# Kernel tuning notes

Measured on AMD Instinct MI355X. Metric: run time of the kernel, lower is better.

The kernel has to match this reference:

```python
import jax, jax.numpy as jnp
import numpy as np

HEADS = 4
DIM_HEAD = 128


def setup_inputs() -> dict:
    key = jax.random.key(0)
    k1, k2, k3, k4 = jax.random.split(key, 4)
    B, C, H, W = 8, 256, 64, 64
    hidden = HEADS * DIM_HEAD  # 512
    x = jax.random.normal(k1, (B, C, H, W), dtype=jnp.float32)
    # 1x1 convs are just channel matmuls; store kernels as [out_ch, in_ch]
    w_qkv = jax.random.normal(k2, (3 * hidden, C), dtype=jnp.float32) * 0.05
    w_out = jax.random.normal(k3, (C, hidden), dtype=jnp.float32) * 0.05
    b_out = jax.random.normal(k4, (C,), dtype=jnp.float32) * 0.05
    return {"x": x, "w_qkv": w_qkv, "w_out": w_out, "b_out": b_out}


def reference(x, w_qkv, w_out, b_out):
    B, C, H, W = x.shape
    n = H * W
    # to_qkv: 1x1 conv without bias == channel matmul
    qkv = jnp.einsum('bchw,oc->bohw', x, w_qkv)  # [B, 3*heads*dim_head, H, W]
    qkv = qkv.reshape(B, 3, HEADS, DIM_HEAD, n)  # 'b (qkv heads c) h w -> b qkv heads c n'
    q, k, v = qkv[:, 0], qkv[:, 1], qkv[:, 2]    # each [B, heads, dim_head, n]
    k = jax.nn.softmax(k, axis=-1)               # softmax over spatial positions
    context = jnp.einsum('bhdn,bhen->bhde', k, v)   # [B, heads, d, e]
    out = jnp.einsum('bhde,bhdn->bhen', context, q)  # [B, heads, e, n]
    out = out.reshape(B, HEADS * DIM_HEAD, H, W)
    # to_out: 1x1 conv with bias
    return jnp.einsum('bchw,oc->bohw', out, w_out) + b_out[None, :, None, None]
```

## Files before the change

### kernel.cpp

```cpp
#include <hip/hip_runtime.h>
#include <stdint.h>


using frag8 = __attribute__((ext_vector_type(8))) short;
using f32x4 = __attribute__((ext_vector_type(4))) float;

__device__ __forceinline__ float bf2f(unsigned short u) {
    union { unsigned int u; float f; } c;
    c.u = ((unsigned int)u) << 16;
    return c.f;
}
__device__ __forceinline__ unsigned short f2bf(float f) {
    union { float f; unsigned int u; } c; c.f = f;
    unsigned int u = c.u;
    return (unsigned short)((u + 0x7FFFu + ((u >> 16) & 1u)) >> 16);
}

__device__ __forceinline__ void gl_lds16(const void* g, void* l) {
    __builtin_amdgcn_global_load_lds(
        (const __attribute__((address_space(1))) unsigned int*)g,
        (__attribute__((address_space(3))) unsigned int*)l, 16, 0, 0);
}

__global__ __launch_bounds__(256) void k0_weights(
    const float* __restrict__ w_qkv, const float* __restrict__ w_out,
    unsigned short* __restrict__ wkvb, unsigned short* __restrict__ woutb,
    unsigned short* __restrict__ wqT)
{
    __shared__ float T[64][65];
    const int blk = blockIdx.x;
    const int tid = threadIdx.x;
    if (blk < 256) {
        const int idx = (blk * 256 + tid) * 4;
        float4 v = *(const float4*)(w_qkv + 512 * 256 + idx);
        ushort4 o;
        o.x = f2bf(v.x); o.y = f2bf(v.y); o.z = f2bf(v.z); o.w = f2bf(v.w);
        *(ushort4*)(wkvb + idx) = o;
    } else if (blk < 384) {
        const int idx = ((blk - 256) * 256 + tid) * 4;
        float4 v = *(const float4*)(w_out + idx);
        ushort4 o;
        o.x = f2bf(v.x); o.y = f2bf(v.y); o.z = f2bf(v.z); o.w = f2bf(v.w);
        *(ushort4*)(woutb + idx) = o;
    } else {
        const int t = blk - 384;
        const int j0 = (t >> 2) * 64, c0 = (t & 3) * 64;
        const int r = tid >> 4, cc = (tid & 15) * 4;
        #pragma unroll
        for (int p = 0; p < 4; ++p) {
            float4 v = *(const float4*)(w_qkv + (j0 + r + p * 16) * 256 + c0 + cc);
            T[r + p * 16][cc + 0] = v.x; T[r + p * 16][cc + 1] = v.y;
            T[r + p * 16][cc + 2] = v.z; T[r + p * 16][cc + 3] = v.w;
        }
        __syncthreads();
        const int c = tid >> 2, jj = (tid & 3) * 16;
        #pragma unroll
        for (int g = 0; g < 4; ++g) {
            ushort4 o;
            o.x = f2bf(T[jj + g * 4 + 0][c]);
            o.y = f2bf(T[jj + g * 4 + 1][c]);
            o.z = f2bf(T[jj + g * 4 + 2][c]);
            o.w = f2bf(T[jj + g * 4 + 3][c]);
            *(ushort4*)(wqT + (c0 + c) * 512 + j0 + jj + g * 4) = o;
        }
    }
}

__global__ __launch_bounds__(256) void k0_xt(
    const float* __restrict__ x, unsigned short* __restrict__ xbT)
{
    __shared__ float T[64][65];
    const int tid = threadIdx.x;
    const int n0 = blockIdx.x * 64, c0 = blockIdx.y * 64, b = blockIdx.z;
    const float* xb = x + (size_t)b * 1048576;
    const int cr = tid >> 4, nc = (tid & 15) * 4;
    #pragma unroll
    for (int p = 0; p < 4; ++p) {
        float4 v = *(const float4*)(xb + (size_t)(c0 + cr + p * 16) * 4096 + n0 + nc);
        T[cr + p * 16][nc + 0] = v.x; T[cr + p * 16][nc + 1] = v.y;
        T[cr + p * 16][nc + 2] = v.z; T[cr + p * 16][nc + 3] = v.w;
    }
    __syncthreads();
    const int n = tid >> 2, cc = (tid & 3) * 16;
    unsigned short* dst = xbT + (size_t)b * 1048576 + (size_t)(n0 + n) * 256 + c0 + cc;
    #pragma unroll
    for (int g = 0; g < 4; ++g) {
        ushort4 o;
        o.x = f2bf(T[cc + g * 4 + 0][n]);
        o.y = f2bf(T[cc + g * 4 + 1][n]);
        o.z = f2bf(T[cc + g * 4 + 2][n]);
        o.w = f2bf(T[cc + g * 4 + 3][n]);
        *(ushort4*)(dst + g * 4) = o;
    }
}

template<int MODE>
__global__ __launch_bounds__(256) void mfma_bt(
    const unsigned short* __restrict__ A0, int lda,
    const unsigned short* __restrict__ B0, int ldb,
    void* __restrict__ C0, int ldc,
    const float* __restrict__ bias, int Kp,
    unsigned long long sAz, unsigned long long sBz, unsigned long long sCz)
{
    __shared__ unsigned short As[128 * 32];
    __shared__ unsigned short Bs[128 * 32];
    const int tid  = threadIdx.x;
    const int w    = tid >> 6, lane = tid & 63;
    const int quad = lane >> 4, l16 = lane & 15;
    const int wm = (w >> 1) * 64, wn = (w & 1) * 64;
    const int z = blockIdx.z;

    const unsigned short* A;
    const unsigned short* B;
    int ks, ke, m0, n0;
    if constexpr (MODE == 2) {
        m0 = 0; n0 = 0;
        ks = blockIdx.x * 512; ke = ks + 512;
        const unsigned long long off =
            ((unsigned long long)(z >> 2) * 1024ull + (unsigned long long)(z & 3) * 128ull) * 4096ull;
        A = A0 + off; B = B0 + off;
    } else if constexpr (MODE == 3) {
        m0 = blockIdx.y * 128; n0 = 0;
        ks = 0; ke = Kp;
        A = A0 + (unsigned long long)(z & 3) * 128ull + (unsigned long long)m0 * lda;
        B = B0 + (unsigned long long)z * 16384ull;
    } else {
        m0 = blockIdx.y * 128; n0 = blockIdx.x * 128;
        ks = 0; ke = Kp;
        A = A0 + sAz * z + (unsigned long long)m0 * lda;
        B = B0 + sBz * z + (unsigned long long)n0 * ldb;
    }

    const int cA0 = w * 128 + lane;
    const int cA1 = cA0 + 64;
    const unsigned short* gA0 = A + (unsigned long long)(cA0 >> 2) * lda + (cA0 & 3) * 8;
    const unsigned short* gA1 = A + (unsigned long long)(cA1 >> 2) * lda + (cA1 & 3) * 8;
    const unsigned short* gB0 = B + (unsigned long long)(cA0 >> 2) * ldb + (cA0 & 3) * 8;
    const unsigned short* gB1 = B + (unsigned long long)(cA1 >> 2) * ldb + (cA1 & 3) * 8;
    unsigned short* lA0 = As + w * 1024;
    unsigned short* lA1 = As + w * 1024 + 512;
    unsigned short* lB0 = Bs + w * 1024;
    unsigned short* lB1 = Bs + w * 1024 + 512;

    f32x4 acc[4][4] = {};

    for (int k0 = ks; k0 < ke; k0 += 32) {
        gl_lds16(gA0 + k0, lA0);
        gl_lds16(gA1 + k0, lA1);
        gl_lds16(gB0 + k0, lB0);
        gl_lds16(gB1 + k0, lB1);
        __syncthreads();
        frag8 a[4], b[4];
        #pragma unroll
        for (int t = 0; t < 4; ++t) {
            a[t] = *(const frag8*)(As + (wm + t * 16 + l16) * 32 + quad * 8);
            b[t] = *(const frag8*)(Bs + (wn + t * 16 + l16) * 32 + quad * 8);
        }
        #pragma unroll
        for (int mt = 0; mt < 4; ++mt)
            #pragma unroll
            for (int nt = 0; nt < 4; ++nt)
                acc[mt][nt] = __builtin_amdgcn_mfma_f32_16x16x32_bf16(
                    a[mt], b[nt], acc[mt][nt], 0, 0, 0);
        __syncthreads();
    }

    if constexpr (MODE == 0 || MODE == 3) {
        unsigned short* C;
        if constexpr (MODE == 0)
            C = (unsigned short*)C0 + sCz * z + (unsigned long long)m0 * ldc + n0;
        else
            C = (unsigned short*)C0 + (unsigned long long)(z >> 2) * 131072ull
              + (unsigned long long)(z & 3) * 128ull + (unsigned long long)m0 * ldc;
        #pragma unroll
        for (int mt = 0; mt < 4; ++mt) {
            const int row = wm + mt * 16 + quad * 4;
            #pragma unroll
            for (int nt = 0; nt < 4; ++nt) {
                const int col = wn + nt * 16 + l16;
                #pragma unroll
                for (int r = 0; r < 4; ++r)
                    C[(unsigned long long)(row + r) * ldc + col] = f2bf(acc[mt][nt][r]);
            }
        }
    } else if constexpr (MODE == 4) {
        unsigned short* C = (unsigned short*)C0 + sCz * z + (unsigned long long)m0 * ldc + n0;
        if (blockIdx.y < 4) {
            float* rs = (float*)bias;
            #pragma unroll
            for (int mt = 0; mt < 4; ++mt) {
                const int row = wm + mt * 16 + quad * 4;
                float rsum[4] = {0.f, 0.f, 0.f, 0.f};
                #pragma unroll
                for (int nt = 0; nt < 4; ++nt) {
                    const int col = wn + nt * 16 + l16;
                    #pragma unroll
                    for (int r = 0; r < 4; ++r) {
                        float e = __expf(acc[mt][nt][r]);
                        rsum[r] += e;
                        C[(unsigned long long)(row + r) * ldc + col] = f2bf(e);
                    }
                }
                #pragma unroll
                for (int r = 0; r < 4; ++r) {
                    float v = rsum[r];
                    v += __shfl_xor(v, 1, 64);
                    v += __shfl_xor(v, 2, 64);
                    v += __shfl_xor(v, 4, 64);
                    v += __shfl_xor(v, 8, 64);
                    if (l16 == 0)
                        atomicAdd(rs + (unsigned long long)z * 512 + m0 + row + r, v);
                }
            }
        } else {
            #pragma unroll
            for (int mt = 0; mt < 4; ++mt) {
                const int row = wm + mt * 16 + quad * 4;
                #pragma unroll
                for (int nt = 0; nt < 4; ++nt) {
                    const int col = wn + nt * 16 + l16;
                    #pragma unroll
                    for (int r = 0; r < 4; ++r)
                        C[(unsigned long long)(row + r) * ldc + col] = f2bf(acc[mt][nt][r]);
                }
            }
        }
    } else if constexpr (MODE == 1) {
        float* C = (float*)C0 + sCz * z + (unsigned long long)m0 * ldc + n0;
        const float* bp = bias + m0;
        #pragma unroll
        for (int mt = 0; mt < 4; ++mt) {
            const int row = wm + mt * 16 + quad * 4;
            #pragma unroll
            for (int nt = 0; nt < 4; ++nt) {
                const int col = wn + nt * 16 + l16;
                #pragma unroll
                for (int r = 0; r < 4; ++r)
                    C[(unsigned long long)(row + r) * ldc + col] = acc[mt][nt][r] + bp[row + r];
            }
        }
    } else {
        float* C = (float*)C0 + (unsigned long long)z * 16384ull;
        #pragma unroll
        for (int mt = 0; mt < 4; ++mt) {
            const int row = wm + mt * 16 + quad * 4;
            #pragma unroll
            for (int nt = 0; nt < 4; ++nt) {
                const int col = wn + nt * 16 + l16;
                #pragma unroll
                for (int r = 0; r < 4; ++r)
                    atomicAdd(C + (row + r) * 128 + col, acc[mt][nt][r]);
            }
        }
    }
}

__global__ __launch_bounds__(256) void k3_scale(
    const float* __restrict__ ctx, const float* __restrict__ rowsum,
    unsigned short* __restrict__ ctxb)
{
    const int idx = (blockIdx.x * 256 + threadIdx.x) * 4;
    const float inv = 1.0f / rowsum[idx >> 7];
    float4 t = *(const float4*)(ctx + idx);
    ushort4 o;
    o.x = f2bf(t.x * inv); o.y = f2bf(t.y * inv);
    o.z = f2bf(t.z * inv); o.w = f2bf(t.w * inv);
    *(ushort4*)(ctxb + idx) = o;
}

extern "C" void kernel_launch(void* const* d_in, const int* in_sizes, int n_in,
                              void* d_out, int out_size, void* d_ws, size_t ws_size,
                              hipStream_t stream) {
    (void)in_sizes; (void)n_in; (void)out_size; (void)ws_size;
    const float* x     = (const float*)d_in[0];
    const float* w_qkv = (const float*)d_in[1];
    const float* w_out = (const float*)d_in[2];
    const float* b_out = (const float*)d_in[3];
    float* out = (float*)d_out;

    char* ws = (char*)d_ws;
    unsigned short* kv     = (unsigned short*)ws;
    unsigned short* xbT    = (unsigned short*)(ws + 67108864);
    unsigned short* wkvb   = (unsigned short*)(ws + 83886080);
    unsigned short* woutb  = (unsigned short*)(ws + 84410368);
    unsigned short* wqT    = (unsigned short*)(ws + 84672512);
    float*          ctx    = (float*)(ws + 84934656);
    float*          rowsum = (float*)(ws + 87031808);
    unsigned short* ctxb   = (unsigned short*)(ws + 87048192);
    unsigned short* Mb     = (unsigned short*)(ws + 88096768);
    unsigned short* Nb     = (unsigned short*)(ws + 90193920);

    hipMemsetAsync(ws + 84934656, 0, 2097152 + 16384, stream);

    k0_weights<<<dim3(416), 256, 0, stream>>>(w_qkv, w_out, wkvb, woutb, wqT);
    k0_xt<<<dim3(64, 4, 8), 256, 0, stream>>>(x, xbT);
    mfma_bt<4><<<dim3(32, 8, 8), 256, 0, stream>>>(
        wkvb, 256, xbT, 256, kv, 4096, rowsum, 256,
        0ull, 1048576ull, 4194304ull);
    mfma_bt<2><<<dim3(8, 1, 32), 256, 0, stream>>>(
        kv, 4096, kv + (size_t)512 * 4096, 4096, ctx, 128, nullptr, 0,
        0ull, 0ull, 0ull);
    k3_scale<<<dim3(512), 256, 0, stream>>>(ctx, rowsum, ctxb);
    mfma_bt<3><<<dim3(1, 2, 32), 256, 0, stream>>>(
        woutb, 512, ctxb, 128, Mb, 512, nullptr, 128,
        0ull, 0ull, 0ull);
    mfma_bt<0><<<dim3(2, 2, 8), 256, 0, stream>>>(
        Mb, 512, wqT, 512, Nb, 256, nullptr, 512,
        131072ull, 0ull, 65536ull);
    mfma_bt<1><<<dim3(32, 2, 8), 256, 0, stream>>>(
        Nb, 256, xbT, 256, out, 4096, b_out, 256,
        65536ull, 1048576ull, 1048576ull);
}
```

Measured before the change: 190.9 us.

## Fuse K/V projection, exp and context GEMM into one kernel; swizzle LDS

Replaces the separate K/V projection kernel (which wrote a 64MB bf16 kv buffer) and the context GEMM with a fused kernel. Each block computes exp(K) and V tiles for 128 spatial positions into LDS, then accumulates K·V^T directly, atomically adding partial context and row sums. It also adds an XOR swizzle to the LDS tile layout in the generic GEMM to reduce bank conflicts. The aim is to remove the large global round trip of kv. In exchange, the fused kernel uses 80KB of LDS, which limits occupancy, and each block recomputes its weight tiles.

After: 200.5 us. 1.05x slower.

```diff
diff --git a/kernel.cpp b/kernel.cpp
--- a/kernel.cpp
+++ b/kernel.cpp
@@ -5,11 +5,6 @@
 using frag8 = __attribute__((ext_vector_type(8))) short;
 using f32x4 = __attribute__((ext_vector_type(4))) float;
 
-__device__ __forceinline__ float bf2f(unsigned short u) {
-    union { unsigned int u; float f; } c;
-    c.u = ((unsigned int)u) << 16;
-    return c.f;
-}
 __device__ __forceinline__ unsigned short f2bf(float f) {
     union { float f; unsigned int u; } c; c.f = f;
     unsigned int u = c.u;
@@ -112,31 +107,24 @@
 
     const unsigned short* A;
     const unsigned short* B;
-    int ks, ke, m0, n0;
-    if constexpr (MODE == 2) {
-        m0 = 0; n0 = 0;
-        ks = blockIdx.x * 512; ke = ks + 512;
-        const unsigned long long off =
-            ((unsigned long long)(z >> 2) * 1024ull + (unsigned long long)(z & 3) * 128ull) * 4096ull;
-        A = A0 + off; B = B0 + off;
-    } else if constexpr (MODE == 3) {
+    int m0, n0;
+    if constexpr (MODE == 3) {
         m0 = blockIdx.y * 128; n0 = 0;
-        ks = 0; ke = Kp;
         A = A0 + (unsigned long long)(z & 3) * 128ull + (unsigned long long)m0 * lda;
         B = B0 + (unsigned long long)z * 16384ull;
     } else {
         m0 = blockIdx.y * 128; n0 = blockIdx.x * 128;
-        ks = 0; ke = Kp;
         A = A0 + sAz * z + (unsigned long long)m0 * lda;
         B = B0 + sBz * z + (unsigned long long)n0 * ldb;
     }
 
-    const int cA0 = w * 128 + lane;
-    const int cA1 = cA0 + 64;
-    const unsigned short* gA0 = A + (unsigned long long)(cA0 >> 2) * lda + (cA0 & 3) * 8;
-    const unsigned short* gA1 = A + (unsigned long long)(cA1 >> 2) * lda + (cA1 & 3) * 8;
-    const unsigned short* gB0 = B + (unsigned long long)(cA0 >> 2) * ldb + (cA0 & 3) * 8;
-    const unsigned short* gB1 = B + (unsigned long long)(cA1 >> 2) * ldb + (cA1 & 3) * 8;
+    const int c0 = w * 128 + lane, c1 = c0 + 64;
+    const int r0 = c0 >> 2, g0 = ((c0 & 3) ^ ((r0 >> 1) & 3)) * 8;
+    const int r1 = c1 >> 2, g1 = ((c1 & 3) ^ ((r1 >> 1) & 3)) * 8;
+    const unsigned short* gA0 = A + (unsigned long long)r0 * lda + g0;
+    const unsigned short* gA1 = A + (unsigned long long)r1 * lda + g1;
+    const unsigned short* gB0 = B + (unsigned long long)r0 * ldb + g0;
+    const unsigned short* gB1 = B + (unsigned long long)r1 * ldb + g1;
     unsigned short* lA0 = As + w * 1024;
     unsigned short* lA1 = As + w * 1024 + 512;
     unsigned short* lB0 = Bs + w * 1024;
@@ -144,7 +132,7 @@
 
     f32x4 acc[4][4] = {};
 
-    for (int k0 = ks; k0 < ke; k0 += 32) {
+    for (int k0 = 0; k0 < Kp; k0 += 32) {
         gl_lds16(gA0 + k0, lA0);
         gl_lds16(gA1 + k0, lA1);
         gl_lds16(gB0 + k0, lB0);
@@ -153,8 +141,10 @@
         frag8 a[4], b[4];
         #pragma unroll
         for (int t = 0; t < 4; ++t) {
-            a[t] = *(const frag8*)(As + (wm + t * 16 + l16) * 32 + quad * 8);
-            b[t] = *(const frag8*)(Bs + (wn + t * 16 + l16) * 32 + quad * 8);
+            const int ra = wm + t * 16 + l16;
+            const int rb = wn + t * 16 + l16;
+            a[t] = *(const frag8*)(As + ra * 32 + ((quad ^ ((ra >> 1) & 3)) << 3));
+            b[t] = *(const frag8*)(Bs + rb * 32 + ((quad ^ ((rb >> 1) & 3)) << 3));
         }
         #pragma unroll
         for (int mt = 0; mt < 4; ++mt)
@@ -183,74 +173,159 @@
                     C[(unsigned long long)(row + r) * ldc + col] = f2bf(acc[mt][nt][r]);
             }
         }
-    } else if constexpr (MODE == 4) {
-        unsigned short* C = (unsigned short*)C0 + sCz * z + (unsigned long long)m0 * ldc + n0;
-        if (blockIdx.y < 4) {
-            float* rs = (float*)bias;
-            #pragma unroll
-            for (int mt = 0; mt < 4; ++mt) {
-                const int row = wm + mt * 16 + quad * 4;
-                float rsum[4] = {0.f, 0.f, 0.f, 0.f};
-                #pragma unroll
-                for (int nt = 0; nt < 4; ++nt) {
-                    const int col = wn + nt * 16 + l16;
+    } else {
+        float* C = (float*)C0 + sCz * z + (unsigned long long)m0 * ldc + n0;
+        const float* bp = bias + m0;
+        #pragma unroll
+        for (int mt = 0; mt < 4; ++mt) {
+            const int row = wm + mt * 16 + quad * 4;
+            #pragma unroll
+            for (int nt = 0; nt < 4; ++nt) {
+                const int col = wn + nt * 16 + l16;
+                #pragma unroll
+                for (int r = 0; r < 4; ++r)
+                    C[(unsigned long long)(row + r) * ldc + col] = acc[mt][nt][r] + bp[row + r];
+            }
+        }
+    }
+}
+
+__global__ __launch_bounds__(256) void k13_ctx(
+    const unsigned short* __restrict__ wkvb,
+    const unsigned short* __restrict__ xbT,
+    float* __restrict__ ctx, float* __restrict__ rowsum)
+{
+    __shared__ unsigned short As[128 * 32];
+    __shared__ unsigned short Bs[128 * 32];
+    __shared__ unsigned short Kt[128 * 128];
+    __shared__ unsigned short Vt[128 * 128];
+    const int tid  = threadIdx.x;
+    const int w    = tid >> 6, lane = tid & 63;
+    const int quad = lane >> 4, l16 = lane & 15;
+    const int wm = (w >> 1) * 64, wn = (w & 1) * 64;
+    const int s = blockIdx.x, h = blockIdx.y, b = blockIdx.z;
+
+    const unsigned short* Wk = wkvb + (size_t)(h * 128) * 256;
+    const unsigned short* Wv = wkvb + (size_t)(512 + h * 128) * 256;
+    const unsigned short* Xb = xbT + (size_t)b * 1048576;
+
+    const int c0 = w * 128 + lane, c1 = c0 + 64;
+    const int r0 = c0 >> 2, g0 = ((c0 & 3) ^ ((r0 >> 1) & 3)) * 8;
+    const int r1 = c1 >> 2, g1 = ((c1 & 3) ^ ((r1 >> 1) & 3)) * 8;
+    unsigned short* lA0 = As + w * 1024;
+    unsigned short* lA1 = As + w * 1024 + 512;
+    unsigned short* lB0 = Bs + w * 1024;
+    unsigned short* lB1 = Bs + w * 1024 + 512;
+
+    float rsum[4][4] = {};
+    f32x4 ctxa[4][4] = {};
+
+    for (int ch = 0; ch < 2; ++ch) {
+        const unsigned short* X0 = Xb + (size_t)(blockIdx.x * 256 + ch * 128) * 256;
+
+        #pragma unroll 1
+        for (int g = 0; g < 2; ++g) {
+            const unsigned short* Wg = g ? Wv : Wk;
+            f32x4 acc[4][4] = {};
+            for (int k0 = 0; k0 < 256; k0 += 32) {
+                gl_lds16(Wg + (size_t)r0 * 256 + g0 + k0, lA0);
+                gl_lds16(Wg + (size_t)r1 * 256 + g1 + k0, lA1);
+                gl_lds16(X0 + (size_t)r0 * 256 + g0 + k0, lB0);
+                gl_lds16(X0 + (size_t)r1 * 256 + g1 + k0, lB1);
+                __syncthreads();
+                frag8 a[4], bb[4];
+                #pragma unroll
+                for (int t = 0; t < 4; ++t) {
+                    const int ra = wm + t * 16 + l16;
+                    const int rb = wn + t * 16 + l16;
+                    a[t]  = *(const frag8*)(As + ra * 32 + ((quad ^ ((ra >> 1) & 3)) << 3));
+                    bb[t] = *(const frag8*)(Bs + rb * 32 + ((quad ^ ((rb >> 1) & 3)) << 3));
+                }
+                #pragma unroll
+                for (int mt = 0; mt < 4; ++mt)
                     #pragma unroll
-                    for (int r = 0; r < 4; ++r) {
-                        float e = __expf(acc[mt][nt][r]);
-                        rsum[r] += e;
-                        C[(unsigned long long)(row + r) * ldc + col] = f2bf(e);
+                    for (int nt = 0; nt < 4; ++nt)
+                        acc[mt][nt] = __builtin_amdgcn_mfma_f32_16x16x32_bf16(
+                            a[mt], bb[nt], acc[mt][nt], 0, 0, 0);
+                __syncthreads();
+            }
+            unsigned short* T = g ? Vt : Kt;
+            if (g == 0) {
+                #pragma unroll
+                for (int mt = 0; mt < 4; ++mt) {
+                    const int row = wm + mt * 16 + quad * 4;
+                    #pragma unroll
+                    for (int nt = 0; nt < 4; ++nt) {
+                        const int col = wn + nt * 16 + l16;
+                        #pragma unroll
+                        for (int r = 0; r < 4; ++r) {
+                            float e = __expf(acc[mt][nt][r]);
+                            rsum[mt][r] += e;
+                            T[((row + r) * 128 + col) ^ (((row + r) & 7) << 3)] = f2bf(e);
+                        }
                     }
                 }
-                #pragma unroll
-                for (int r = 0; r < 4; ++r) {
-                    float v = rsum[r];
-                    v += __shfl_xor(v, 1, 64);
-                    v += __shfl_xor(v, 2, 64);
-                    v += __shfl_xor(v, 4, 64);
-                    v += __shfl_xor(v, 8, 64);
-                    if (l16 == 0)
-                        atomicAdd(rs + (unsigned long long)z * 512 + m0 + row + r, v);
+            } else {
+                #pragma unroll
+                for (int mt = 0; mt < 4; ++mt) {
+                    const int row = wm + mt * 16 + quad * 4;
+                    #pragma unroll
+                    for (int nt = 0; nt < 4; ++nt) {
+                        const int col = wn + nt * 16 + l16;
+                        #pragma unroll
+                        for (int r = 0; r < 4; ++r)
+                            T[((row + r) * 128 + col) ^ (((row + r) & 7) << 3)] =
+                                f2bf(acc[mt][nt][r]);
+                    }
                 }
             }
-        } else {
-            #pragma unroll
-            for (int mt = 0; mt < 4; ++mt) {
-                const int row = wm + mt * 16 + quad * 4;
-                #pragma unroll
-                for (int nt = 0; nt < 4; ++nt) {
-                    const int col = wn + nt * 16 + l16;
-                    #pragma unroll
-                    for (int r = 0; r < 4; ++r)
-                        C[(unsigned long long)(row + r) * ldc + col] = f2bf(acc[mt][nt][r]);
-                }
-            }
-        }
-    } else if constexpr (MODE == 1) {
-        float* C = (float*)C0 + sCz * z + (unsigned long long)m0 * ldc + n0;
-        const float* bp = bias + m0;
-        #pragma unroll
-        for (int mt = 0; mt < 4; ++mt) {
-            const int row = wm + mt * 16 + quad * 4;
-            #pragma unroll
-            for (int nt = 0; nt < 4; ++nt) {
-                const int col = wn + nt * 16 + l16;
-                #pragma unroll
-                for (int r = 0; r < 4; ++r)
-                    C[(unsigned long long)(row + r) * ldc + col] = acc[mt][nt][r] + bp[row + r];
-            }
-        }
-    } else {
-        float* C = (float*)C0 + (unsigned long long)z * 16384ull;
-        #pragma unroll
-        for (int mt = 0; mt < 4; ++mt) {
-            const int row = wm + mt * 16 + quad * 4;
-            #pragma unroll
-            for (int nt = 0; nt < 4; ++nt) {
-                const int col = wn + nt * 16 + l16;
-                #pragma unroll
-                for (int r = 0; r < 4; ++r)
-                    atomicAdd(C + (row + r) * 128 + col, acc[mt][nt][r]);
-            }
+        }
+        __syncthreads();
+
+        #pragma unroll
+        for (int kk = 0; kk < 4; ++kk) {
+            frag8 a[4], bb[4];
+            #pragma unroll
+            for (int t = 0; t < 4; ++t) {
+                const int ra = wm + t * 16 + l16;
+                const int rb = wn + t * 16 + l16;
+                a[t]  = *(const frag8*)(Kt + ((ra * 128 + kk * 32 + quad * 8) ^ ((ra & 7) << 3)));
+                bb[t] = *(const frag8*)(Vt + ((rb * 128 + kk * 32 + quad * 8) ^ ((rb & 7) << 3)));
+            }
+            #pragma unroll
+            for (int mt = 0; mt < 4; ++mt)
+                #pragma unroll
+                for (int nt = 0; nt < 4; ++nt)
+                    ctxa[mt][nt] = __builtin_amdgcn_mfma_f32_16x16x32_bf16(
+                        a[mt], bb[nt], ctxa[mt][nt], 0, 0, 0);
+        }
+        __syncthreads();
+    }
+
+    float* cp = ctx + (size_t)(b * 4 + h) * 16384ull;
+    #pragma unroll
+    for (int mt = 0; mt < 4; ++mt) {
+        const int row = wm + mt * 16 + quad * 4;
+        #pragma unroll
+        for (int nt = 0; nt < 4; ++nt) {
+            const int col = wn + nt * 16 + l16;
+            #pragma unroll
+            for (int r = 0; r < 4; ++r)
+                atomicAdd(cp + (row + r) * 128 + col, ctxa[mt][nt][r]);
+        }
+    }
+    float* rs = rowsum + b * 512 + h * 128;
+    #pragma unroll
+    for (int mt = 0; mt < 4; ++mt) {
+        const int row = wm + mt * 16 + quad * 4;
+        #pragma unroll
+        for (int r = 0; r < 4; ++r) {
+            float v = rsum[mt][r];
+            v += __shfl_xor(v, 1, 64);
+            v += __shfl_xor(v, 2, 64);
+            v += __shfl_xor(v, 4, 64);
+            v += __shfl_xor(v, 8, 64);
+            if (l16 == 0) atomicAdd(rs + row + r, v);
         }
     }
 }
@@ -279,27 +354,21 @@
     float* out = (float*)d_out;
 
     char* ws = (char*)d_ws;
-    unsigned short* kv     = (unsigned short*)ws;
-    unsigned short* xbT    = (unsigned short*)(ws + 67108864);
-    unsigned short* wkvb   = (unsigned short*)(ws + 83886080);
-    unsigned short* woutb  = (unsigned short*)(ws + 84410368);
-    unsigned short* wqT    = (unsigned short*)(ws + 84672512);
-    float*          ctx    = (float*)(ws + 84934656);
-    float*          rowsum = (float*)(ws + 87031808);
-    unsigned short* ctxb   = (unsigned short*)(ws + 87048192);
-    unsigned short* Mb     = (unsigned short*)(ws + 88096768);
-    unsigned short* Nb     = (unsigned short*)(ws + 90193920);
-
-    hipMemsetAsync(ws + 84934656, 0, 2097152 + 16384, stream);
+    unsigned short* xbT    = (unsigned short*)ws;
+    unsigned short* wkvb   = (unsigned short*)(ws + 16777216);
+    unsigned short* woutb  = (unsigned short*)(ws + 17301504);
+    unsigned short* wqT    = (unsigned short*)(ws + 17563648);
+    float*          ctx    = (float*)(ws + 17825792);
+    float*          rowsum = (float*)(ws + 19922944);
+    unsigned short* ctxb   = (unsigned short*)(ws + 19939328);
+    unsigned short* Mb     = (unsigned short*)(ws + 20987904);
+    unsigned short* Nb     = (unsigned short*)(ws + 23085056);
+
+    hipMemsetAsync(ws + 17825792, 0, 2097152 + 16384, stream);
 
     k0_weights<<<dim3(416), 256, 0, stream>>>(w_qkv, w_out, wkvb, woutb, wqT);
     k0_xt<<<dim3(64, 4, 8), 256, 0, stream>>>(x, xbT);
-    mfma_bt<4><<<dim3(32, 8, 8), 256, 0, stream>>>(
-        wkvb, 256, xbT, 256, kv, 4096, rowsum, 256,
-        0ull, 1048576ull, 4194304ull);
-    mfma_bt<2><<<dim3(8, 1, 32), 256, 0, stream>>>(
-        kv, 4096, kv + (size_t)512 * 4096, 4096, ctx, 128, nullptr, 0,
-        0ull, 0ull, 0ull);
+    k13_ctx<<<dim3(16, 4, 8), 256, 0, stream>>>(wkvb, xbT, ctx, rowsum);
     k3_scale<<<dim3(512), 256, 0, stream>>>(ctx, rowsum, ctxb);
     mfma_bt<3><<<dim3(1, 2, 32), 256, 0, stream>>>(
         woutb, 512, ctxb, 128, Mb, 512, nullptr, 128,
```

## Swizzle LDS tiles, replace ctx atomics with split-K partials, fuse prep kernels

Applied to the files above, without the earlier changes.

Applies an XOR swizzle to the LDS tile layout in the shared MFMA GEMM so that fragment reads avoid bank conflicts. The split-K context GEMM now writes per-slice partial buffers instead of issuing float atomics, and the scale kernel sums the eight slices before normalising. The weight-conversion and x-transpose kernels are merged into one launch, and the memset shrinks to cover only rowsum. This costs extra partial-buffer traffic (16 MB written and read) in exchange for removing atomics and one launch.

After: 184.5 us. 1.03x faster.

```diff
diff --git a/kernel.cpp b/kernel.cpp
--- a/kernel.cpp
+++ b/kernel.cpp
@@ -5,11 +5,6 @@
 using frag8 = __attribute__((ext_vector_type(8))) short;
 using f32x4 = __attribute__((ext_vector_type(4))) float;
 
-__device__ __forceinline__ float bf2f(unsigned short u) {
-    union { unsigned int u; float f; } c;
-    c.u = ((unsigned int)u) << 16;
-    return c.f;
-}
 __device__ __forceinline__ unsigned short f2bf(float f) {
     union { float f; unsigned int u; } c; c.f = f;
     unsigned int u = c.u;
@@ -22,14 +17,40 @@
         (__attribute__((address_space(3))) unsigned int*)l, 16, 0, 0);
 }
 
-__global__ __launch_bounds__(256) void k0_weights(
-    const float* __restrict__ w_qkv, const float* __restrict__ w_out,
-    unsigned short* __restrict__ wkvb, unsigned short* __restrict__ woutb,
-    unsigned short* __restrict__ wqT)
+__global__ __launch_bounds__(256) void k0_prep(
+    const float* __restrict__ x, const float* __restrict__ w_qkv,
+    const float* __restrict__ w_out,
+    unsigned short* __restrict__ xbT, unsigned short* __restrict__ wkvb,
+    unsigned short* __restrict__ woutb, unsigned short* __restrict__ wqT)
 {
     __shared__ float T[64][65];
-    const int blk = blockIdx.x;
     const int tid = threadIdx.x;
+    const int blk0 = blockIdx.x;
+    if (blk0 < 2048) {
+        const int n0 = (blk0 & 63) * 64, c0 = ((blk0 >> 6) & 3) * 64, b = blk0 >> 8;
+        const float* xb = x + (size_t)b * 1048576;
+        const int cr = tid >> 4, nc = (tid & 15) * 4;
+        #pragma unroll
+        for (int p = 0; p < 4; ++p) {
+            float4 v = *(const float4*)(xb + (size_t)(c0 + cr + p * 16) * 4096 + n0 + nc);
+            T[cr + p * 16][nc + 0] = v.x; T[cr + p * 16][nc + 1] = v.y;
+            T[cr + p * 16][nc + 2] = v.z; T[cr + p * 16][nc + 3] = v.w;
+        }
+        __syncthreads();
+        const int n = tid >> 2, cc = (tid & 3) * 16;
+        unsigned short* dst = xbT + (size_t)b * 1048576 + (size_t)(n0 + n) * 256 + c0 + cc;
+        #pragma unroll
+        for (int g = 0; g < 4; ++g) {
+            ushort4 o;
+            o.x = f2bf(T[cc + g * 4 + 0][n]);
+            o.y = f2bf(T[cc + g * 4 + 1][n]);
+            o.z = f2bf(T[cc + g * 4 + 2][n]);
+            o.w = f2bf(T[cc + g * 4 + 3][n]);
+            *(ushort4*)(dst + g * 4) = o;
+        }
+        return;
+    }
+    const int blk = blk0 - 2048;
     if (blk < 256) {
         const int idx = (blk * 256 + tid) * 4;
         float4 v = *(const float4*)(w_qkv + 512 * 256 + idx);
@@ -66,34 +87,6 @@
     }
 }
 
-__global__ __launch_bounds__(256) void k0_xt(
-    const float* __restrict__ x, unsigned short* __restrict__ xbT)
-{
-    __shared__ float T[64][65];
-    const int tid = threadIdx.x;
-    const int n0 = blockIdx.x * 64, c0 = blockIdx.y * 64, b = blockIdx.z;
-    const float* xb = x + (size_t)b * 1048576;
-    const int cr = tid >> 4, nc = (tid & 15) * 4;
-    #pragma unroll
-    for (int p = 0; p < 4; ++p) {
-        float4 v = *(const float4*)(xb + (size_t)(c0 + cr + p * 16) * 4096 + n0 + nc);
-        T[cr + p * 16][nc + 0] = v.x; T[cr + p * 16][nc + 1] = v.y;
-        T[cr + p * 16][nc + 2] = v.z; T[cr + p * 16][nc + 3] = v.w;
-    }
-    __syncthreads();
-    const int n = tid >> 2, cc = (tid & 3) * 16;
-    unsigned short* dst = xbT + (size_t)b * 1048576 + (size_t)(n0 + n) * 256 + c0 + cc;
-    #pragma unroll
-    for (int g = 0; g < 4; ++g) {
-        ushort4 o;
-        o.x = f2bf(T[cc + g * 4 + 0][n]);
-        o.y = f2bf(T[cc + g * 4 + 1][n]);
-        o.z = f2bf(T[cc + g * 4 + 2][n]);
-        o.w = f2bf(T[cc + g * 4 + 3][n]);
-        *(ushort4*)(dst + g * 4) = o;
-    }
-}
-
 template<int MODE>
 __global__ __launch_bounds__(256) void mfma_bt(
     const unsigned short* __restrict__ A0, int lda,
@@ -112,31 +105,32 @@
 
     const unsigned short* A;
     const unsigned short* B;
-    int ks, ke, m0, n0;
+    int m0, n0, ks, NS;
     if constexpr (MODE == 2) {
         m0 = 0; n0 = 0;
-        ks = blockIdx.x * 512; ke = ks + 512;
+        ks = blockIdx.x * 512; NS = 16;
         const unsigned long long off =
             ((unsigned long long)(z >> 2) * 1024ull + (unsigned long long)(z & 3) * 128ull) * 4096ull;
         A = A0 + off; B = B0 + off;
     } else if constexpr (MODE == 3) {
         m0 = blockIdx.y * 128; n0 = 0;
-        ks = 0; ke = Kp;
+        ks = 0; NS = Kp >> 5;
         A = A0 + (unsigned long long)(z & 3) * 128ull + (unsigned long long)m0 * lda;
         B = B0 + (unsigned long long)z * 16384ull;
     } else {
         m0 = blockIdx.y * 128; n0 = blockIdx.x * 128;
-        ks = 0; ke = Kp;
+        ks = 0; NS = Kp >> 5;
         A = A0 + sAz * z + (unsigned long long)m0 * lda;
         B = B0 + sBz * z + (unsigned long long)n0 * ldb;
     }
 
-    const int cA0 = w * 128 + lane;
-    const int cA1 = cA0 + 64;
-    const unsigned short* gA0 = A + (unsigned long long)(cA0 >> 2) * lda + (cA0 & 3) * 8;
-    const unsigned short* gA1 = A + (unsigned long long)(cA1 >> 2) * lda + (cA1 & 3) * 8;
-    const unsigned short* gB0 = B + (unsigned long long)(cA0 >> 2) * ldb + (cA0 & 3) * 8;
-    const unsigned short* gB1 = B + (unsigned long long)(cA1 >> 2) * ldb + (cA1 & 3) * 8;
+    const int c0 = w * 128 + lane, c1 = c0 + 64;
+    const int r0 = c0 >> 2, s0 = ((c0 & 3) ^ ((r0 >> 1) & 3)) * 8;
+    const int r1 = c1 >> 2, s1 = ((c1 & 3) ^ ((r1 >> 1) & 3)) * 8;
+    const unsigned short* gA0 = A + (unsigned long long)r0 * lda + s0 + ks;
+    const unsigned short* gA1 = A + (unsigned long long)r1 * lda + s1 + ks;
+    const unsigned short* gB0 = B + (unsigned long long)r0 * ldb + s0 + ks;
+    const unsigned short* gB1 = B + (unsigned long long)r1 * ldb + s1 + ks;
     unsigned short* lA0 = As + w * 1024;
     unsigned short* lA1 = As + w * 1024 + 512;
     unsigned short* lB0 = Bs + w * 1024;
@@ -144,7 +138,8 @@
 
     f32x4 acc[4][4] = {};
 
-    for (int k0 = ks; k0 < ke; k0 += 32) {
+    for (int t = 0; t < NS; ++t) {
+        const int k0 = t * 32;
         gl_lds16(gA0 + k0, lA0);
         gl_lds16(gA1 + k0, lA1);
         gl_lds16(gB0 + k0, lB0);
@@ -152,9 +147,11 @@
         __syncthreads();
         frag8 a[4], b[4];
         #pragma unroll
-        for (int t = 0; t < 4; ++t) {
-            a[t] = *(const frag8*)(As + (wm + t * 16 + l16) * 32 + quad * 8);
-            b[t] = *(const frag8*)(Bs + (wn + t * 16 + l16) * 32 + quad * 8);
+        for (int tt = 0; tt < 4; ++tt) {
+            const int ra = wm + tt * 16 + l16;
+            const int rb = wn + tt * 16 + l16;
+            a[tt] = *(const frag8*)(As + ra * 32 + ((quad ^ ((ra >> 1) & 3)) << 3));
+            b[tt] = *(const frag8*)(Bs + rb * 32 + ((quad ^ ((rb >> 1) & 3)) << 3));
         }
         #pragma unroll
         for (int mt = 0; mt < 4; ++mt)
@@ -240,7 +237,7 @@
             }
         }
     } else {
-        float* C = (float*)C0 + (unsigned long long)z * 16384ull;
+        float* C = (float*)C0 + ((unsigned long long)blockIdx.x * 32 + z) * 16384ull;
         #pragma unroll
         for (int mt = 0; mt < 4; ++mt) {
             const int row = wm + mt * 16 + quad * 4;
@@ -249,22 +246,27 @@
                 const int col = wn + nt * 16 + l16;
                 #pragma unroll
                 for (int r = 0; r < 4; ++r)
-                    atomicAdd(C + (row + r) * 128 + col, acc[mt][nt][r]);
-            }
-        }
-    }
-}
-
-__global__ __launch_bounds__(256) void k3_scale(
-    const float* __restrict__ ctx, const float* __restrict__ rowsum,
+                    C[(row + r) * 128 + col] = acc[mt][nt][r];
+            }
+        }
+    }
+}
+
+__global__ __launch_bounds__(256) void k3_sumscale(
+    const float* __restrict__ ctxp, const float* __restrict__ rowsum,
     unsigned short* __restrict__ ctxb)
 {
     const int idx = (blockIdx.x * 256 + threadIdx.x) * 4;
+    float4 s = make_float4(0.f, 0.f, 0.f, 0.f);
+    #pragma unroll
+    for (int sl = 0; sl < 8; ++sl) {
+        float4 t = *(const float4*)(ctxp + (size_t)sl * 524288 + idx);
+        s.x += t.x; s.y += t.y; s.z += t.z; s.w += t.w;
+    }
     const float inv = 1.0f / rowsum[idx >> 7];
-    float4 t = *(const float4*)(ctx + idx);
     ushort4 o;
-    o.x = f2bf(t.x * inv); o.y = f2bf(t.y * inv);
-    o.z = f2bf(t.z * inv); o.w = f2bf(t.w * inv);
+    o.x = f2bf(s.x * inv); o.y = f2bf(s.y * inv);
+    o.z = f2bf(s.z * inv); o.w = f2bf(s.w * inv);
     *(ushort4*)(ctxb + idx) = o;
 }
 
@@ -279,28 +281,27 @@
     float* out = (float*)d_out;
 
     char* ws = (char*)d_ws;
-    unsigned short* kv     = (unsigned short*)ws;
-    unsigned short* xbT    = (unsigned short*)(ws + 67108864);
-    unsigned short* wkvb   = (unsigned short*)(ws + 83886080);
-    unsigned short* woutb  = (unsigned short*)(ws + 84410368);
-    unsigned short* wqT    = (unsigned short*)(ws + 84672512);
-    float*          ctx    = (float*)(ws + 84934656);
-    float*          rowsum = (float*)(ws + 87031808);
-    unsigned short* ctxb   = (unsigned short*)(ws + 87048192);
-    unsigned short* Mb     = (unsigned short*)(ws + 88096768);
-    unsigned short* Nb     = (unsigned short*)(ws + 90193920);
-
-    hipMemsetAsync(ws + 84934656, 0, 2097152 + 16384, stream);
-
-    k0_weights<<<dim3(416), 256, 0, stream>>>(w_qkv, w_out, wkvb, woutb, wqT);
-    k0_xt<<<dim3(64, 4, 8), 256, 0, stream>>>(x, xbT);
+    unsigned short* xbT    = (unsigned short*)ws;
+    unsigned short* wkvb   = (unsigned short*)(ws + 16777216);
+    unsigned short* woutb  = (unsigned short*)(ws + 17301504);
+    unsigned short* wqT    = (unsigned short*)(ws + 17563648);
+    float*          ctxp   = (float*)(ws + 17825792);
+    float*          rowsum = (float*)(ws + 34603008);
+    unsigned short* ctxb   = (unsigned short*)(ws + 34619392);
+    unsigned short* Mb     = (unsigned short*)(ws + 35667968);
+    unsigned short* Nb     = (unsigned short*)(ws + 37765120);
+    unsigned short* kv     = (unsigned short*)(ws + 38813696);
+
+    hipMemsetAsync(ws + 34603008, 0, 16384, stream);
+
+    k0_prep<<<dim3(2464), 256, 0, stream>>>(x, w_qkv, w_out, xbT, wkvb, woutb, wqT);
     mfma_bt<4><<<dim3(32, 8, 8), 256, 0, stream>>>(
         wkvb, 256, xbT, 256, kv, 4096, rowsum, 256,
         0ull, 1048576ull, 4194304ull);
     mfma_bt<2><<<dim3(8, 1, 32), 256, 0, stream>>>(
-        kv, 4096, kv + (size_t)512 * 4096, 4096, ctx, 128, nullptr, 0,
+        kv, 4096, kv + (size_t)512 * 4096, 4096, ctxp, 128, nullptr, 0,
         0ull, 0ull, 0ull);
-    k3_scale<<<dim3(512), 256, 0, stream>>>(ctx, rowsum, ctxb);
+    k3_sumscale<<<dim3(512), 256, 0, stream>>>(ctxp, rowsum, ctxb);
     mfma_bt<3><<<dim3(1, 2, 32), 256, 0, stream>>>(
         woutb, 512, ctxb, 128, Mb, 512, nullptr, 128,
         0ull, 0ull, 0ull);
```
